# Optimization experiments

Hardware: AMD Instinct MI355X
Metric: run time of the kernel (lower is better)

Reference implementation:

```python
import jax, jax.numpy as jnp
import numpy as np

N_NODES = 100000
N_EDGES = 3200000
N_GRAPHS = 128
F_IN, HID, N_CLS = 3, 64, 6


def setup_inputs() -> dict:
    key = jax.random.key(0)
    ks = jax.random.split(key, 9)
    x = jax.random.normal(ks[0], (N_NODES, F_IN), dtype=jnp.float32)
    edge_index = jax.random.randint(ks[1], (2, N_EDGES), 0, N_NODES, dtype=jnp.int32)
    batch = jnp.sort(jax.random.randint(ks[2], (N_NODES,), 0, N_GRAPHS, dtype=jnp.int32))
    # GCNConv weights (glorot-ish) and biases
    W1 = jax.random.normal(ks[3], (F_IN, HID), dtype=jnp.float32) / np.float32(np.sqrt(F_IN))
    b1 = jnp.zeros((HID,), dtype=jnp.float32)
    W2 = jax.random.normal(ks[4], (HID, HID), dtype=jnp.float32) / np.float32(np.sqrt(HID))
    b2 = jnp.zeros((HID,), dtype=jnp.float32)
    Wl = jax.random.normal(ks[5], (HID, N_CLS), dtype=jnp.float32) / np.float32(np.sqrt(HID))
    bl = jnp.zeros((N_CLS,), dtype=jnp.float32)
    return {"x": x, "edge_index": edge_index, "batch": batch,
            "W1": W1, "b1": b1, "W2": W2, "b2": b2, "Wl": Wl, "bl": bl}


def _gcn_forward(x, edge_index, batch, W1, b1, W2, b2, Wl, bl):
    n = x.shape[0]
    # add self-loops (PyG GCNConv default)
    loop = jnp.arange(n, dtype=edge_index.dtype)
    src = jnp.concatenate([edge_index[0], loop])
    dst = jnp.concatenate([edge_index[1], loop])
    # symmetric normalization D^{-1/2} (A+I) D^{-1/2}
    deg = jax.ops.segment_sum(jnp.ones_like(dst, dtype=x.dtype), dst, num_segments=n)
    dis = jax.lax.rsqrt(jnp.maximum(deg, 1.0))
    norm = dis[src] * dis[dst]  # [E+N]

    def conv(h, W, b):
        h = h @ W                                   # [N, out]
        msg = h[src] * norm[:, None]                # gather + scale
        agg = jax.ops.segment_sum(msg, dst, num_segments=n)  # scatter-add
        return agg + b

    h = jax.nn.relu(conv(x, W1, b1))
    h = jax.nn.relu(conv(h, W2, b2))
    # global mean pool over graphs
    ones = jnp.ones((n,), dtype=h.dtype)
    cnt = jax.ops.segment_sum(ones, batch, num_segments=N_GRAPHS)
    pooled = jax.ops.segment_sum(h, batch, num_segments=N_GRAPHS) / jnp.maximum(cnt, 1.0)[:, None]
    logits = pooled @ Wl + bl
    return jax.nn.log_softmax(logits, axis=1)


def reference(x, edge_index, batch, W1, b1, W2, b2, Wl, bl):
    return _gcn_forward(x, edge_index, batch, W1, b1, W2, b2, Wl, bl)
```

## Files before the change

kernel.cpp:

```cpp
#include <hip/hip_runtime.h>
#include <math.h>

#define NGRAPH 128
#define NPB 128
#define CAPB 6144
#define PSL 8
#define MMN 16
#define TILEA 16384
#define EPTA 16


__device__ inline unsigned char f2fp8(float f) {
    float a = fabsf(f);
    unsigned s = (__float_as_uint(f) >> 31) << 7;
    if (!(a > 0.f)) return (unsigned char)s;
    if (a >= 448.f) return (unsigned char)(s | 0x7e);
    int e = (int)(__float_as_uint(a) >> 23) - 127;
    if (e < -6) e = -6;
    float sc = __uint_as_float((unsigned)(130 - e) << 23);
    int q = (int)rintf(a * sc);
    if (q >= 16) { e += 1; q = 8; }
    if (q <= 0) return (unsigned char)s;
    unsigned expb, man;
    if (q < 8) { expb = 0; man = (unsigned)q; }
    else { expb = (unsigned)(e + 7); man = (unsigned)(q - 8); }
    return (unsigned char)(s | (expb << 3) | man);
}

typedef float v2f __attribute__((ext_vector_type(2)));

__device__ inline void fp8x4_dec(unsigned u, float* o) {
#pragma unroll
    for (int k = 0; k < 4; ++k) {
        unsigned b = (u >> (8 * k)) & 0xffu;
        unsigned bits = ((b & 0x80u) << 24) | ((b & 0x7fu) << 20);
        o[k] = __uint_as_float(bits) * 0x1p+120f;
    }
}

__device__ inline void acc16(uint4 u, float w, v2f* a) {
#if __has_builtin(__builtin_amdgcn_cvt_pk_f32_fp8)
    v2f ws; ws.x = w; ws.y = w;
    a[0] += __builtin_amdgcn_cvt_pk_f32_fp8(u.x, false) * ws;
    a[1] += __builtin_amdgcn_cvt_pk_f32_fp8(u.x, true)  * ws;
    a[2] += __builtin_amdgcn_cvt_pk_f32_fp8(u.y, false) * ws;
    a[3] += __builtin_amdgcn_cvt_pk_f32_fp8(u.y, true)  * ws;
    a[4] += __builtin_amdgcn_cvt_pk_f32_fp8(u.z, false) * ws;
    a[5] += __builtin_amdgcn_cvt_pk_f32_fp8(u.z, true)  * ws;
    a[6] += __builtin_amdgcn_cvt_pk_f32_fp8(u.w, false) * ws;
    a[7] += __builtin_amdgcn_cvt_pk_f32_fp8(u.w, true)  * ws;
#else
    float* af = (float*)a;
    unsigned uu[4] = {u.x, u.y, u.z, u.w};
#pragma unroll
    for (int q = 0; q < 4; ++q) {
        float d[4]; fp8x4_dec(uu[q], d);
#pragma unroll
        for (int k = 0; k < 4; ++k) af[q * 4 + k] += d[k] * w;
    }
#endif
}


__global__ void init_k(int* __restrict__ cursorF, float* __restrict__ pooled, int NBF) {
    int i = blockIdx.x * blockDim.x + threadIdx.x;
    if (i < NBF) cursorF[i] = i * CAPB;
    if (i < NGRAPH * 64) pooled[i] = 0.0f;
}


__global__ __launch_bounds__(1024) void binA_k(const int* __restrict__ src,
        const int* __restrict__ dst, int* cursorF, unsigned* __restrict__ binned,
        int E, int NBF) {
    __shared__ int lh[1024];
    int tid = threadIdx.x;
    lh[tid] = 0;
    __syncthreads();
    int base = blockIdx.x * TILEA;
    int d[EPTA];
#pragma unroll
    for (int u = 0; u < EPTA; ++u) {
        int e = base + tid + u * 1024;
        d[u] = (e < E) ? dst[e] : -1;
    }
#pragma unroll
    for (int u = 0; u < EPTA; ++u)
        if (d[u] >= 0) atomicAdd(&lh[d[u] >> 7], 1);
    __syncthreads();
    if (tid < NBF) {
        int cnt = lh[tid];
        lh[tid] = cnt ? atomicAdd(&cursorF[tid], cnt) : 0;
    }
    __syncthreads();
#pragma unroll
    for (int u = 0; u < EPTA; ++u) {
        if (d[u] >= 0) {
            int e = base + tid + u * 1024;
            int p = atomicAdd(&lh[d[u] >> 7], 1);
            binned[p] = (unsigned)src[e] | ((unsigned)(d[u] & (NPB - 1)) << 17);
        }
    }
}


__global__ __launch_bounds__(256) void reorder_k(unsigned* __restrict__ binned,
        const int* __restrict__ cursorF, int* __restrict__ nodebeg,
        int* __restrict__ nodeend, float* __restrict__ dis, int n) {
    __shared__ int hist[NPB + 1];
    __shared__ int startv[NPB + 1];
    __shared__ unsigned lout[CAPB];
    int tid = threadIdx.x;
    int b = blockIdx.x;
    int beg = b * CAPB, end = cursorF[b];
    int total = end - beg;
    if (tid <= NPB) hist[tid] = 0;
    __syncthreads();
    for (int i = beg + tid; i < end; i += 256)
        atomicAdd(&hist[binned[i] >> 17], 1);
    __syncthreads();
    if (tid < NPB) startv[tid + 1] = hist[tid];
    if (tid == 0) startv[0] = 0;
    __syncthreads();
    for (int off = 1; off <= NPB; off <<= 1) {
        int v = 0;
        if (tid <= NPB && tid >= off) v = startv[tid - off];
        __syncthreads();
        if (tid <= NPB && tid >= off) startv[tid] += v;
        __syncthreads();
    }
    if (tid < NPB) hist[tid] = startv[tid];
    __syncthreads();
    for (int i = beg + tid; i < end; i += 256) {
        unsigned r = binned[i];
        int p = atomicAdd(&hist[r >> 17], 1);
        lout[p] = r & 0x1FFFFu;
    }
    __syncthreads();
    for (int jj = tid; jj < total; jj += 256)
        binned[beg + jj] = lout[jj];
    int node0 = b * NPB;
    if (tid < NPB) {
        int node = node0 + tid;
        if (node < n) {
            nodebeg[node] = beg + startv[tid];
            nodeend[node] = beg + startv[tid + 1];
            int deg = startv[tid + 1] - startv[tid];
            dis[node] = rsqrtf((float)deg + 1.0f);
        }
    }
}


__global__ __launch_bounds__(256) void mm12_k(const float* __restrict__ x,
        const int* __restrict__ nodebeg, const int* __restrict__ nodeend,
        const int* __restrict__ csr, const float* __restrict__ dis,
        const float* __restrict__ W1, const float* __restrict__ b1,
        const float* __restrict__ W2, unsigned char* __restrict__ tb, int n) {
    __shared__ __attribute__((aligned(16))) float hrow[4][64];
    __shared__ float4 ytile[MMN];
    int tid = threadIdx.x;
    int j = tid & 63;

    float w1r0 = W1[j], w1r1 = W1[64 + j], w1r2 = W1[128 + j], bbr = b1[j];
    float wreg[64];
#pragma unroll
    for (int k = 0; k < 64; ++k) wreg[k] = W2[k * 64 + j];

    int ns = tid >> 4;
    int el = tid & 15;
    int gnode = blockIdx.x * MMN + ns;
    float a0 = 0.f, a1 = 0.f, a2 = 0.f;
    float dn = 0.f;
    int b = 0, e = 0;
    if (gnode < n) {
        dn = dis[gnode];
        b = nodebeg[gnode];
        e = nodeend[gnode];
    }
    for (int i = b + el; i < e; i += 32) {
        int s0 = csr[i];
        int i1 = i + 16;
        bool v1 = i1 < e;
        int s1 = v1 ? csr[i1] : s0;
        float w0 = dis[s0];
        float w1e = v1 ? dis[s1] : 0.f;
        float p0 = x[s0 * 3], p1 = x[s0 * 3 + 1], p2 = x[s0 * 3 + 2];
        float q0 = x[s1 * 3], q1 = x[s1 * 3 + 1], q2 = x[s1 * 3 + 2];
        a0 += p0 * w0 + q0 * w1e;
        a1 += p1 * w0 + q1 * w1e;
        a2 += p2 * w0 + q2 * w1e;
    }
#pragma unroll
    for (int off = 1; off <= 8; off <<= 1) {
        a0 += __shfl_xor(a0, off);
        a1 += __shfl_xor(a1, off);
        a2 += __shfl_xor(a2, off);
    }
    if (el == 0 && gnode < n) {
        float xs0 = x[gnode * 3], xs1 = x[gnode * 3 + 1], xs2 = x[gnode * 3 + 2];
        ytile[ns] = make_float4(dn * (a0 + dn * xs0),
                                dn * (a1 + dn * xs1),
                                dn * (a2 + dn * xs2), 0.f);
    }
    __syncthreads();

    int nl = tid >> 6;
    for (int it = 0; it < MMN / 4; ++it) {
        int slot = it * 4 + nl;
        int node = blockIdx.x * MMN + slot;
        float4 yv = ytile[slot];
        float h = fmaxf(yv.x * w1r0 + yv.y * w1r1 + yv.z * w1r2 + bbr, 0.0f);
        hrow[nl][j] = h;
        __builtin_amdgcn_wave_barrier();
        float acc = 0.0f;
#pragma unroll
        for (int k = 0; k < 64; k += 4) {
            float4 h4 = *(const float4*)&hrow[nl][k];
            acc += h4.x * wreg[k + 0];
            acc += h4.y * wreg[k + 1];
            acc += h4.z * wreg[k + 2];
            acc += h4.w * wreg[k + 3];
        }
        if (node < n) tb[node * 64 + j] = f2fp8(acc);
        __builtin_amdgcn_wave_barrier();
    }
}


__global__ __launch_bounds__(256) void gather2_k(const unsigned char* __restrict__ tb,
        const float* __restrict__ b2, const int* __restrict__ nodebeg,
        const int* __restrict__ nodeend, const int* __restrict__ csr,
        const float* __restrict__ dis, float* __restrict__ agg, int n) {
    int g = blockIdx.x * blockDim.x + threadIdx.x;
    int node = g >> 6;
    if (node >= n) return;
    int lane = threadIdx.x & 63;
    int c4 = lane & 3, esub = lane >> 2;
    const uint4* t16 = (const uint4*)tb;
    float dn = dis[node];
    float dnn = dn * dn;
    int b = nodebeg[node], e = nodeend[node];
    v2f av[8];
#pragma unroll
    for (int k = 0; k < 8; ++k) { av[k].x = 0.f; av[k].y = 0.f; }
    for (int i = b; i < e + 1; i += 48) {
        int i0 = i + esub, i1 = i0 + 16, i2 = i0 + 32;
        int s0 = (i0 < e) ? csr[i0] : node;
        int s1 = (i1 < e) ? csr[i1] : node;
        int s2 = (i2 < e) ? csr[i2] : node;
        float w0 = (i0 < e) ? dis[s0] * dn : ((i0 == e) ? dnn : 0.f);
        float w1 = (i1 < e) ? dis[s1] * dn : ((i1 == e) ? dnn : 0.f);
        float w2 = (i2 < e) ? dis[s2] * dn : ((i2 == e) ? dnn : 0.f);
        uint4 u0 = t16[s0 * 4 + c4];
        uint4 u1 = t16[s1 * 4 + c4];
        uint4 u2 = t16[s2 * 4 + c4];
        acc16(u0, w0, av);
        acc16(u1, w1, av);
        acc16(u2, w2, av);
    }
    float* a = (float*)av;
    {
        bool hi = (esub & 1) != 0;
#pragma unroll
        for (int t = 0; t < 8; ++t) {
            float send = hi ? a[t] : a[8 + t];
            float r = __shfl_xor(send, 4);
            a[t] = (hi ? a[8 + t] : a[t]) + r;
        }
    }
    {
        bool hi = (esub & 2) != 0;
#pragma unroll
        for (int t = 0; t < 4; ++t) {
            float send = hi ? a[t] : a[4 + t];
            float r = __shfl_xor(send, 8);
            a[t] = (hi ? a[4 + t] : a[t]) + r;
        }
    }
    {
        bool hi = (esub & 4) != 0;
#pragma unroll
        for (int t = 0; t < 2; ++t) {
            float send = hi ? a[t] : a[2 + t];
            float r = __shfl_xor(send, 16);
            a[t] = (hi ? a[2 + t] : a[t]) + r;
        }
    }
    {
        bool hi = (esub & 8) != 0;
        float send = hi ? a[0] : a[1];
        float r = __shfl_xor(send, 32);
        a[0] = (hi ? a[1] : a[0]) + r;
    }
    int chan = ((esub & 1) << 3) | ((esub & 2) << 1) | ((esub & 4) >> 1) | ((esub & 8) >> 3);
    agg[node * 64 + c4 * 16 + chan] = a[0] + b2[c4 * 16 + chan];
}


__device__ inline int lower_bound_i(const int* a, int n, int key) {
    int lo = 0, hi = n;
    while (lo < hi) {
        int mid = (lo + hi) >> 1;
        if (a[mid] < key) lo = mid + 1; else hi = mid;
    }
    return lo;
}

__global__ void pool_k(const float* __restrict__ agg2, const int* __restrict__ batch,
                       float* __restrict__ pooled, int n) {
    int g = blockIdx.x / PSL, slice = blockIdx.x % PSL;
    int start = lower_bound_i(batch, n, g);
    int end   = lower_bound_i(batch, n, g + 1);
    int len = end - start;
    int cb = start + (int)(((long long)len * slice) / PSL);
    int ce = start + (int)(((long long)len * (slice + 1)) / PSL);
    int wid = threadIdx.x >> 6, lane = threadIdx.x & 63;
    float acc = 0.0f;
    for (int i = cb + wid; i < ce; i += 4)
        acc += fmaxf(agg2[i * 64 + lane], 0.0f);
    __shared__ float red[4][64];
    red[wid][lane] = acc;
    __syncthreads();
    if (threadIdx.x < 64) {
        float s = red[0][lane] + red[1][lane] + red[2][lane] + red[3][lane];
        atomicAdd(&pooled[g * 64 + lane], s);
    }
}

__global__ void head_k(const float* __restrict__ pooled, const int* __restrict__ batch,
                       const float* __restrict__ Wl, const float* __restrict__ bl,
                       float* __restrict__ out, int n) {
    int g = blockIdx.x, t = threadIdx.x;
    __shared__ float p[64];
    __shared__ float logit[8];
    int start = lower_bound_i(batch, n, g);
    int end   = lower_bound_i(batch, n, g + 1);
    float cnt = fmaxf((float)(end - start), 1.0f);
    p[t] = pooled[g * 64 + t] / cnt;
    __syncthreads();
    if (t < 6) {
        float a = bl[t];
        for (int k = 0; k < 64; ++k) a += p[k] * Wl[k * 6 + t];
        logit[t] = a;
    }
    __syncthreads();
    if (t == 0) {
        float m = logit[0];
        for (int j = 1; j < 6; ++j) m = fmaxf(m, logit[j]);
        float s = 0.0f;
        for (int j = 0; j < 6; ++j) s += expf(logit[j] - m);
        float lse = m + logf(s);
        for (int j = 0; j < 6; ++j) out[g * 6 + j] = logit[j] - lse;
    }
}


extern "C" void kernel_launch(void* const* d_in, const int* in_sizes, int n_in,
                              void* d_out, int out_size, void* d_ws, size_t ws_size,
                              hipStream_t stream) {
    const float* x     = (const float*)d_in[0];
    const int*   ei    = (const int*)d_in[1];
    const int*   batch = (const int*)d_in[2];
    const float* W1    = (const float*)d_in[3];
    const float* b1    = (const float*)d_in[4];
    const float* W2    = (const float*)d_in[5];
    const float* b2    = (const float*)d_in[6];
    const float* Wl    = (const float*)d_in[7];
    const float* bl    = (const float*)d_in[8];

    int n = in_sizes[0] / 3;
    int E = in_sizes[1] / 2;
    const int* src = ei;
    const int* dst = ei + E;

    int NBF = (n + NPB - 1) / NPB;
    int GA = (E + TILEA - 1) / TILEA;

    char* ws = (char*)d_ws;
    size_t o = 0;
    auto alloc = [&](size_t bytes) -> void* {
        void* p = ws + o;
        o += (bytes + 255) & ~(size_t)255;
        return p;
    };
    int*      cursorF = (int*)alloc((size_t)NBF * 4);
    float*    dis     = (float*)alloc((size_t)n * 4);
    int*      nodebeg = (int*)alloc((size_t)n * 4);
    int*      nodeend = (int*)alloc((size_t)n * 4);
    float*    pooled  = (float*)alloc((size_t)NGRAPH * 64 * 4);
    unsigned* binned  = (unsigned*)alloc((size_t)NBF * CAPB * 4);
    unsigned char* tb = (unsigned char*)alloc((size_t)n * 64);
    float*    agg     = (float*)alloc((size_t)n * 64 * 4);
    float*    out = (float*)d_out;

    int initN = NGRAPH * 64;
    init_k<<<(initN + 255) / 256, 256, 0, stream>>>(cursorF, pooled, NBF);
    binA_k<<<GA, 1024, 0, stream>>>(src, dst, cursorF, binned, E, NBF);
    reorder_k<<<NBF, 256, 0, stream>>>(binned, cursorF, nodebeg, nodeend, dis, n);

    mm12_k<<<(n + MMN - 1) / MMN, 256, 0, stream>>>(x, nodebeg, nodeend,
            (const int*)binned, dis, W1, b1, W2, tb, n);
    gather2_k<<<(n * 64 + 255) / 256, 256, 0, stream>>>(tb, b2, nodebeg, nodeend,
            (const int*)binned, dis, agg, n);

    pool_k<<<NGRAPH * PSL, 256, 0, stream>>>(agg, batch, pooled, n);
    head_k<<<NGRAPH, 64, 0, stream>>>(pooled, batch, Wl, bl, out, n);
}
```

Before: 249.5 us.

## Fold source-side normalization into features to drop per-edge dis gathers

Precomputes x scaled by dis in the reorder kernel and folds the source-side dis factor into the fp8 layer-2 table, so both gather kernels no longer load dis[src] per edge. The destination dis is applied once per node after aggregation. It also unrolls the layer-2 gather to four edges per iteration and halves the binning tile with 512-thread blocks. The cost is an extra small xs buffer, and fp8 now quantizes the pre-scaled values, which slightly changes rounding.

```diff
diff --git a/kernel.cpp b/kernel.cpp
--- a/kernel.cpp
+++ b/kernel.cpp
@@ -6,7 +6,7 @@
 #define CAPB 6144
 #define PSL 8
 #define MMN 16
-#define TILEA 16384
+#define TILEA 8192
 #define EPTA 16
 
 
@@ -69,33 +69,34 @@
 }
 
 
-__global__ __launch_bounds__(1024) void binA_k(const int* __restrict__ src,
+__global__ __launch_bounds__(512) void binA_k(const int* __restrict__ src,
         const int* __restrict__ dst, int* cursorF, unsigned* __restrict__ binned,
         int E, int NBF) {
     __shared__ int lh[1024];
     int tid = threadIdx.x;
     lh[tid] = 0;
+    lh[tid + 512] = 0;
     __syncthreads();
     int base = blockIdx.x * TILEA;
     int d[EPTA];
 #pragma unroll
     for (int u = 0; u < EPTA; ++u) {
-        int e = base + tid + u * 1024;
+        int e = base + tid + u * 512;
         d[u] = (e < E) ? dst[e] : -1;
     }
 #pragma unroll
     for (int u = 0; u < EPTA; ++u)
         if (d[u] >= 0) atomicAdd(&lh[d[u] >> 7], 1);
     __syncthreads();
-    if (tid < NBF) {
-        int cnt = lh[tid];
-        lh[tid] = cnt ? atomicAdd(&cursorF[tid], cnt) : 0;
+    for (int t = tid; t < NBF; t += 512) {
+        int cnt = lh[t];
+        lh[t] = cnt ? atomicAdd(&cursorF[t], cnt) : 0;
     }
     __syncthreads();
 #pragma unroll
     for (int u = 0; u < EPTA; ++u) {
         if (d[u] >= 0) {
-            int e = base + tid + u * 1024;
+            int e = base + tid + u * 512;
             int p = atomicAdd(&lh[d[u] >> 7], 1);
             binned[p] = (unsigned)src[e] | ((unsigned)(d[u] & (NPB - 1)) << 17);
         }
@@ -105,7 +106,8 @@
 
 __global__ __launch_bounds__(256) void reorder_k(unsigned* __restrict__ binned,
         const int* __restrict__ cursorF, int* __restrict__ nodebeg,
-        int* __restrict__ nodeend, float* __restrict__ dis, int n) {
+        int* __restrict__ nodeend, float* __restrict__ dis,
+        const float* __restrict__ x, float* __restrict__ xs, int n) {
     __shared__ int hist[NPB + 1];
     __shared__ int startv[NPB + 1];
     __shared__ unsigned lout[CAPB];
@@ -145,13 +147,17 @@
             nodebeg[node] = beg + startv[tid];
             nodeend[node] = beg + startv[tid + 1];
             int deg = startv[tid + 1] - startv[tid];
-            dis[node] = rsqrtf((float)deg + 1.0f);
-        }
-    }
-}
-
-
-__global__ __launch_bounds__(256) void mm12_k(const float* __restrict__ x,
+            float d = rsqrtf((float)deg + 1.0f);
+            dis[node] = d;
+            xs[node * 3]     = x[node * 3] * d;
+            xs[node * 3 + 1] = x[node * 3 + 1] * d;
+            xs[node * 3 + 2] = x[node * 3 + 2] * d;
+        }
+    }
+}
+
+
+__global__ __launch_bounds__(256) void mm12_k(const float* __restrict__ xs,
         const int* __restrict__ nodebeg, const int* __restrict__ nodeend,
         const int* __restrict__ csr, const float* __restrict__ dis,
         const float* __restrict__ W1, const float* __restrict__ b1,
@@ -182,13 +188,12 @@
         int i1 = i + 16;
         bool v1 = i1 < e;
         int s1 = v1 ? csr[i1] : s0;
-        float w0 = dis[s0];
-        float w1e = v1 ? dis[s1] : 0.f;
-        float p0 = x[s0 * 3], p1 = x[s0 * 3 + 1], p2 = x[s0 * 3 + 2];
-        float q0 = x[s1 * 3], q1 = x[s1 * 3 + 1], q2 = x[s1 * 3 + 2];
-        a0 += p0 * w0 + q0 * w1e;
-        a1 += p1 * w0 + q1 * w1e;
-        a2 += p2 * w0 + q2 * w1e;
+        float m1 = v1 ? 1.f : 0.f;
+        float p0 = xs[s0 * 3], p1 = xs[s0 * 3 + 1], p2 = xs[s0 * 3 + 2];
+        float q0 = xs[s1 * 3], q1 = xs[s1 * 3 + 1], q2 = xs[s1 * 3 + 2];
+        a0 += p0 + q0 * m1;
+        a1 += p1 + q1 * m1;
+        a2 += p2 + q2 * m1;
     }
 #pragma unroll
     for (int off = 1; off <= 8; off <<= 1) {
@@ -197,10 +202,9 @@
         a2 += __shfl_xor(a2, off);
     }
     if (el == 0 && gnode < n) {
-        float xs0 = x[gnode * 3], xs1 = x[gnode * 3 + 1], xs2 = x[gnode * 3 + 2];
-        ytile[ns] = make_float4(dn * (a0 + dn * xs0),
-                                dn * (a1 + dn * xs1),
-                                dn * (a2 + dn * xs2), 0.f);
+        ytile[ns] = make_float4(dn * (a0 + xs[gnode * 3]),
+                                dn * (a1 + xs[gnode * 3 + 1]),
+                                dn * (a2 + xs[gnode * 3 + 2]), dn);
     }
     __syncthreads();
 
@@ -221,7 +225,7 @@
             acc += h4.z * wreg[k + 2];
             acc += h4.w * wreg[k + 3];
         }
-        if (node < n) tb[node * 64 + j] = f2fp8(acc);
+        if (node < n) tb[node * 64 + j] = f2fp8(acc * yv.w);
         __builtin_amdgcn_wave_barrier();
     }
 }
@@ -238,25 +242,28 @@
     int c4 = lane & 3, esub = lane >> 2;
     const uint4* t16 = (const uint4*)tb;
     float dn = dis[node];
-    float dnn = dn * dn;
     int b = nodebeg[node], e = nodeend[node];
     v2f av[8];
 #pragma unroll
     for (int k = 0; k < 8; ++k) { av[k].x = 0.f; av[k].y = 0.f; }
-    for (int i = b; i < e + 1; i += 48) {
-        int i0 = i + esub, i1 = i0 + 16, i2 = i0 + 32;
+    for (int i = b; i < e + 1; i += 64) {
+        int i0 = i + esub, i1 = i0 + 16, i2 = i0 + 32, i3 = i0 + 48;
         int s0 = (i0 < e) ? csr[i0] : node;
         int s1 = (i1 < e) ? csr[i1] : node;
         int s2 = (i2 < e) ? csr[i2] : node;
-        float w0 = (i0 < e) ? dis[s0] * dn : ((i0 == e) ? dnn : 0.f);
-        float w1 = (i1 < e) ? dis[s1] * dn : ((i1 == e) ? dnn : 0.f);
-        float w2 = (i2 < e) ? dis[s2] * dn : ((i2 == e) ? dnn : 0.f);
+        int s3 = (i3 < e) ? csr[i3] : node;
+        float w0 = (i0 <= e) ? 1.f : 0.f;
+        float w1 = (i1 <= e) ? 1.f : 0.f;
+        float w2 = (i2 <= e) ? 1.f : 0.f;
+        float w3 = (i3 <= e) ? 1.f : 0.f;
         uint4 u0 = t16[s0 * 4 + c4];
         uint4 u1 = t16[s1 * 4 + c4];
         uint4 u2 = t16[s2 * 4 + c4];
+        uint4 u3 = t16[s3 * 4 + c4];
         acc16(u0, w0, av);
         acc16(u1, w1, av);
         acc16(u2, w2, av);
+        acc16(u3, w3, av);
     }
     float* a = (float*)av;
     {
@@ -293,7 +300,7 @@
         a[0] = (hi ? a[1] : a[0]) + r;
     }
     int chan = ((esub & 1) << 3) | ((esub & 2) << 1) | ((esub & 4) >> 1) | ((esub & 8) >> 3);
-    agg[node * 64 + c4 * 16 + chan] = a[0] + b2[c4 * 16 + chan];
+    agg[node * 64 + c4 * 16 + chan] = dn * a[0] + b2[c4 * 16 + chan];
 }
 
 
@@ -387,6 +394,7 @@
     float*    dis     = (float*)alloc((size_t)n * 4);
     int*      nodebeg = (int*)alloc((size_t)n * 4);
     int*      nodeend = (int*)alloc((size_t)n * 4);
+    float*    xs      = (float*)alloc((size_t)n * 3 * 4);
     float*    pooled  = (float*)alloc((size_t)NGRAPH * 64 * 4);
     unsigned* binned  = (unsigned*)alloc((size_t)NBF * CAPB * 4);
     unsigned char* tb = (unsigned char*)alloc((size_t)n * 64);
@@ -395,10 +403,10 @@
 
     int initN = NGRAPH * 64;
     init_k<<<(initN + 255) / 256, 256, 0, stream>>>(cursorF, pooled, NBF);
-    binA_k<<<GA, 1024, 0, stream>>>(src, dst, cursorF, binned, E, NBF);
-    reorder_k<<<NBF, 256, 0, stream>>>(binned, cursorF, nodebeg, nodeend, dis, n);
-
-    mm12_k<<<(n + MMN - 1) / MMN, 256, 0, stream>>>(x, nodebeg, nodeend,
+    binA_k<<<GA, 512, 0, stream>>>(src, dst, cursorF, binned, E, NBF);
+    reorder_k<<<NBF, 256, 0, stream>>>(binned, cursorF, nodebeg, nodeend, dis, x, xs, n);
+
+    mm12_k<<<(n + MMN - 1) / MMN, 256, 0, stream>>>(xs, nodebeg, nodeend,
             (const int*)binned, dis, W1, b1, W2, tb, n);
     gather2_k<<<(n * 64 + 255) / 256, 256, 0, stream>>>(tb, b2, nodebeg, nodeend,
             (const int*)binned, dis, agg, n);
```

Result: faster. 239.5 us (-4.0%).
